# Kernel tuning notes

Measured on AMD Instinct MI355X. Metric: run time of the kernel, lower is better.

## Reference

```python
import jax, jax.numpy as jnp
import numpy as np

B, N, C = 2, 20000, 128
E = 320000
H, COUT = 4, 64
HD = 256  # hidden_dim == H*COUT -> projection is None
ED = 16
L = 3  # LSTM layers


def setup_inputs() -> dict:
    key = jax.random.key(0)
    ks = jax.random.split(key, 16)
    return {
        "x": jax.random.normal(ks[0], (B, N, C), jnp.float32),
        "edge_index": jax.random.randint(ks[1], (2, E), 0, N),
        "edge_attr": jax.random.normal(ks[2], (E, ED), jnp.float32),
        "lin_w": jax.random.normal(ks[3], (C, H * COUT), jnp.float32) / np.sqrt(C),
        "att_src": jax.random.normal(ks[4], (1, H, COUT), jnp.float32) * 0.1,
        "att_dst": jax.random.normal(ks[5], (1, H, COUT), jnp.float32) * 0.1,
        "lin_edge_w": jax.random.normal(ks[6], (ED, H * COUT), jnp.float32) / np.sqrt(ED),
        "att_edge": jax.random.normal(ks[7], (1, H, COUT), jnp.float32) * 0.1,
        "gat_bias": jnp.zeros((H * COUT,), jnp.float32),
        "w_ih": jax.random.normal(ks[8], (L, 4 * HD, HD), jnp.float32) / np.sqrt(HD),
        "w_hh": jax.random.normal(ks[9], (L, 4 * HD, HD), jnp.float32) / np.sqrt(HD),
        "b_ih": jnp.zeros((L, 4 * HD), jnp.float32),
        "b_hh": jnp.zeros((L, 4 * HD), jnp.float32),
        "ln_g": jnp.ones((HD,), jnp.float32),
        "ln_b": jnp.zeros((HD,), jnp.float32),
    }


def reference(x, edge_index, edge_attr, lin_w, att_src, att_dst, lin_edge_w,
              att_edge, gat_bias, w_ih, w_hh, b_ih, b_hh, ln_g, ln_b):
    Bn = B * N
    # ---- GAT: linear transform ----
    xt = (x.reshape(Bn, C) @ lin_w).reshape(Bn, H, COUT)
    # batch-offset edge index, then append self-loops for every node
    off = (jnp.arange(B, dtype=edge_index.dtype) * N)[:, None]
    src = (edge_index[0][None, :] + off).reshape(-1)
    dst = (edge_index[1][None, :] + off).reshape(-1)
    loop = jnp.arange(Bn, dtype=edge_index.dtype)
    src = jnp.concatenate([src, loop])  # [Etot] = [B*E + B*N]
    dst = jnp.concatenate([dst, loop])
    # edge features: shared 2D edge_attr is repeated per batch, zeros on self-loops
    ea = (edge_attr @ lin_edge_w).reshape(E, H, COUT)
    ea = jnp.concatenate([jnp.tile(ea, (B, 1, 1)),
                          jnp.zeros((Bn, H, COUT), xt.dtype)], axis=0)
    # ---- message: gather, score, segment-softmax ----
    x_j = xt[src]  # [Etot, H, COUT]
    x_i = xt[dst]
    alpha = ((x_j * att_src).sum(-1) + (x_i * att_dst).sum(-1)
             + (ea * att_edge).sum(-1))  # [Etot, H]
    alpha = jax.nn.leaky_relu(alpha, 0.2)
    m = jax.ops.segment_max(alpha, dst, num_segments=Bn)
    alpha = jnp.exp(alpha - m[dst])
    s = jax.ops.segment_sum(alpha, dst, num_segments=Bn)
    alpha = alpha / (s[dst] + 1e-16)  # PyG softmax eps; dropout inactive (eval)
    # ---- aggregate (scatter-add) ----
    out = jax.ops.segment_sum(x_j * alpha[..., None], dst, num_segments=Bn)
    spatial = out.reshape(Bn, H * COUT) + gat_bias  # concat heads, [Bn, HD]
    # ---- 3-layer LSTM, seq_len=1, zero initial state (h_prev=None) ----
    h_in = spatial
    hs, cs = [], []
    for l in range(L):
        # h0 = c0 = 0 -> w_hh contributes nothing; inter-layer dropout inactive
        gates = h_in @ w_ih[l].T + b_ih[l] + b_hh[l]
        i, f, g, o = jnp.split(gates, 4, axis=-1)  # PyTorch gate order i,f,g,o
        c = jax.nn.sigmoid(i) * jnp.tanh(g)
        h = jax.nn.sigmoid(o) * jnp.tanh(c)
        hs.append(h)
        cs.append(c)
        h_in = h
    # ---- LayerNorm ----
    h_out = h_in.reshape(B, N, HD)
    mu = h_out.mean(-1, keepdims=True)
    var = ((h_out - mu) ** 2).mean(-1, keepdims=True)
    h_out = (h_out - mu) / jnp.sqrt(var + 1e-5) * ln_g + ln_b
    return h_out, jnp.stack(hs), jnp.stack(cs)
```

## Files before the change

### kernel.cpp

```cpp
#include <hip/hip_runtime.h>
#include <stdint.h>

#define NB_    20000
#define CB_    128
#define EE_    320000
#define BN_    40000
#define BE_    640000
#define ETOT_  680000

typedef __attribute__((ext_vector_type(4))) float f4;
typedef __attribute__((ext_vector_type(4))) unsigned short us4;
typedef __attribute__((ext_vector_type(4))) unsigned int ui4;
typedef __attribute__((ext_vector_type(8))) __bf16 bf16x8;

static __device__ __forceinline__ unsigned short f2bf(float f){
    union { float f; unsigned int u; } v; v.f = f;
    unsigned int u = v.u;
    u += 0x7FFFu + ((u >> 16) & 1u);
    return (unsigned short)(u >> 16);
}
static __device__ __forceinline__ float bf2f(unsigned short b){
    union { unsigned int u; float f; } v; v.u = ((unsigned int)b) << 16;
    return v.f;
}
static __device__ __forceinline__ float sigf(float x){ return 1.f/(1.f+__expf(-x)); }
static __device__ __forceinline__ float tanhfast(float x){ return 2.f/(1.f+__expf(-2.f*x)) - 1.f; }
static __device__ __forceinline__ f4 fmax4(f4 a, f4 b){
    f4 r; r[0]=fmaxf(a[0],b[0]); r[1]=fmaxf(a[1],b[1]); r[2]=fmaxf(a[2],b[2]); r[3]=fmaxf(a[3],b[3]); return r;
}

__global__ void w2_kernel(const float* __restrict__ lew, const float* __restrict__ ae,
                          float* __restrict__ W2){
    int t = threadIdx.x;
    int d = t >> 2, h = t & 3;
    float s = 0.f;
    for (int c = 0; c < 64; ++c) s += lew[d*256 + h*64 + c] * ae[h*64 + c];
    W2[d*4 + h] = s;
}

__global__ void pack_linwT_kernel(const float* __restrict__ lw, unsigned short* __restrict__ wt){
    int tid = blockIdx.x*256 + threadIdx.x;
    int n = tid >> 7, k = tid & 127;
    wt[n*128 + k] = f2bf(lw[k*256 + n]);
}

__global__ void pack_lstmw_kernel(const float* __restrict__ w_ih, unsigned short* __restrict__ Bp){
    int tid = blockIdx.x*256 + threadIdx.x;
    int l   = tid / 196608;
    int rem = tid - l*196608;
    int p = rem >> 8, k = rem & 255;
    int jb = p / 192, q2 = p - jb*192;
    int chunk = q2 / 48, r = q2 - chunk*48;
    int gate = r >> 4, jj = r & 15;
    int gor = (gate == 0) ? 0 : (gate == 1 ? 2 : 3);
    int srcrow = gor*256 + jb*64 + chunk*16 + jj;
    Bp[tid] = f2bf(w_ih[(l*1024 + srcrow)*256 + k]);
}

__global__ void pack_bias_kernel(const float* __restrict__ b_ih, const float* __restrict__ b_hh,
                                 float* __restrict__ bp){
    int tid = blockIdx.x*256 + threadIdx.x;
    if (tid >= 2304) return;
    int l = tid / 768, p = tid - l*768;
    int jb = p / 192, q2 = p - jb*192;
    int chunk = q2 / 48, r = q2 - chunk*48;
    int gate = r >> 4, jj = r & 15;
    int gor = (gate == 0) ? 0 : (gate == 1 ? 2 : 3);
    int srcrow = gor*256 + jb*64 + chunk*16 + jj;
    bp[tid] = b_ih[l*1024 + srcrow] + b_hh[l*1024 + srcrow];
}

__global__ __launch_bounds__(256) void gemm1_kernel(const float* __restrict__ x,
        const unsigned short* __restrict__ wt, unsigned short* __restrict__ xt){
    __shared__ unsigned short As[64*72];
    __shared__ unsigned short Bs[64*72];
    const int tid = threadIdx.x;
    const int bm = blockIdx.x, bn = blockIdx.y;
    const int lane = tid & 63, w = tid >> 6;
    const int wm = w & 1, wn = w >> 1;
    const int nl = lane & 15, q = lane >> 4;
    f4 acc[2][2] = {};
    for (int kc = 0; kc < 128; kc += 64) {
        #pragma unroll
        for (int it = 0; it < 4; ++it) {
            int s = tid + it*256;
            int row = s >> 4, c4 = s & 15;
            f4 v = *(const f4*)&x[(bm*64+row)*128 + kc + c4*4];
            us4 o; o[0]=f2bf(v[0]); o[1]=f2bf(v[1]); o[2]=f2bf(v[2]); o[3]=f2bf(v[3]);
            *(us4*)&As[row*72 + c4*4] = o;
        }
        #pragma unroll
        for (int it = 0; it < 2; ++it) {
            int s = tid + it*256;
            int row = s >> 3, c = s & 7;
            *(ui4*)&Bs[row*72 + c*8] = *(const ui4*)&wt[(bn*64+row)*128 + kc + c*8];
        }
        __syncthreads();
        #pragma unroll
        for (int kk = 0; kk < 64; kk += 32) {
            bf16x8 a[2], b[2];
            #pragma unroll
            for (int mt = 0; mt < 2; ++mt) a[mt] = *(const bf16x8*)&As[(wm*32 + mt*16 + nl)*72 + kk + q*8];
            #pragma unroll
            for (int nt = 0; nt < 2; ++nt) b[nt] = *(const bf16x8*)&Bs[(wn*32 + nt*16 + nl)*72 + kk + q*8];
            #pragma unroll
            for (int mt = 0; mt < 2; ++mt)
                #pragma unroll
                for (int nt = 0; nt < 2; ++nt)
                    acc[mt][nt] = __builtin_amdgcn_mfma_f32_16x16x32_bf16(a[mt], b[nt], acc[mt][nt], 0, 0, 0);
        }
        __syncthreads();
    }
    #pragma unroll
    for (int mt = 0; mt < 2; ++mt)
        #pragma unroll
        for (int nt = 0; nt < 2; ++nt)
            #pragma unroll
            for (int r = 0; r < 4; ++r) {
                int row = bm*64 + wm*32 + mt*16 + q*4 + r;
                int col = bn*64 + wn*32 + nt*16 + nl;
                xt[row*256 + col] = f2bf(acc[mt][nt][r]);
            }
}

__global__ __launch_bounds__(256) void scores_kernel(const unsigned short* __restrict__ xt,
        const float* __restrict__ att_src, const float* __restrict__ att_dst,
        float* __restrict__ s_src, float* __restrict__ s_dst){
    int n = blockIdx.x*4 + (threadIdx.x >> 6);
    int lane = threadIdx.x & 63;
    us4 xv = *(const us4*)&xt[n*256 + lane*4];
    f4 as = *(const f4*)&att_src[lane*4];
    f4 ad = *(const f4*)&att_dst[lane*4];
    float x0=bf2f(xv[0]), x1=bf2f(xv[1]), x2=bf2f(xv[2]), x3=bf2f(xv[3]);
    float ps = x0*as[0]+x1*as[1]+x2*as[2]+x3*as[3];
    float pd = x0*ad[0]+x1*ad[1]+x2*ad[2]+x3*ad[3];
    #pragma unroll
    for (int o = 1; o < 16; o <<= 1) { ps += __shfl_xor(ps, o, 64); pd += __shfl_xor(pd, o, 64); }
    if ((lane & 15) == 0) {
        s_src[n*4 + (lane>>4)] = ps;
        s_dst[n*4 + (lane>>4)] = pd;
    }
}

__global__ __launch_bounds__(256) void eascore_kernel(const float* __restrict__ ea,
        const float* __restrict__ W2, float* __restrict__ esc){
    __shared__ float w2s[64];
    if (threadIdx.x < 64) w2s[threadIdx.x] = W2[threadIdx.x];
    __syncthreads();
    int e = blockIdx.x*256 + threadIdx.x;
    if (e >= EE_) return;
    f4 acc = {};
    #pragma unroll
    for (int d = 0; d < 16; ++d) {
        float v = ea[e*16 + d];
        f4 wv = *(const f4*)&w2s[d*4];
        acc += v * wv;
    }
    *(f4*)&esc[e*4] = acc;
}

__global__ __launch_bounds__(256) void deghist_kernel(const int* __restrict__ ei, int* __restrict__ deg){
    int e = blockIdx.x*256 + threadIdx.x;
    if (e >= ETOT_) return;
    int dst;
    if (e < BE_) { int b = e / EE_, ee = e - b*EE_; dst = ei[EE_ + ee] + b*NB_; }
    else dst = e - BE_;
    atomicAdd(&deg[dst], 1);
}

__global__ __launch_bounds__(256) void scan1_kernel(const int* __restrict__ deg,
        int* __restrict__ inc, int* __restrict__ bsum){
    __shared__ int sd[256];
    int t = threadIdx.x, i = blockIdx.x*256 + t;
    int v = (i < BN_) ? deg[i] : 0;
    sd[t] = v; __syncthreads();
    #pragma unroll
    for (int d = 1; d < 256; d <<= 1) {
        int x = (t >= d) ? sd[t-d] : 0; __syncthreads();
        sd[t] += x; __syncthreads();
    }
    inc[i] = sd[t];
    if (t == 255) bsum[blockIdx.x] = sd[255];
}

__global__ __launch_bounds__(256) void scan2_kernel(const int* __restrict__ bsum,
        int* __restrict__ bpre, int nb){
    __shared__ int sd[256];
    int t = threadIdx.x;
    int v = (t < nb) ? bsum[t] : 0;
    sd[t] = v; __syncthreads();
    #pragma unroll
    for (int d = 1; d < 256; d <<= 1) {
        int x = (t >= d) ? sd[t-d] : 0; __syncthreads();
        sd[t] += x; __syncthreads();
    }
    if (t < nb) bpre[t] = sd[t] - v;
}

__global__ __launch_bounds__(256) void scan3_kernel(const int* __restrict__ inc,
        const int* __restrict__ deg, const int* __restrict__ bpre,
        int* __restrict__ offs, int* __restrict__ cur){
    int i = blockIdx.x*256 + threadIdx.x;
    if (i >= BN_) return;
    int o = inc[i] - deg[i] + bpre[blockIdx.x];
    offs[i] = o; cur[i] = o;
}

__global__ __launch_bounds__(256) void scatter_kernel(const int* __restrict__ ei,
        const float* __restrict__ s_src, const float* __restrict__ s_dst,
        const float* __restrict__ esc, int* __restrict__ cur,
        int* __restrict__ csr_src, float* __restrict__ csr_alpha){
    int e = blockIdx.x*256 + threadIdx.x;
    if (e >= ETOT_) return;
    int src, dst; f4 a;
    if (e < BE_) {
        int b = e / EE_, ee = e - b*EE_;
        src = ei[ee] + b*NB_;
        dst = ei[EE_ + ee] + b*NB_;
        a = *(const f4*)&esc[ee*4];
    } else {
        src = dst = e - BE_;
        a = (f4){0.f, 0.f, 0.f, 0.f};
    }
    a += *(const f4*)&s_src[src*4];
    a += *(const f4*)&s_dst[dst*4];
    #pragma unroll
    for (int h = 0; h < 4; ++h) a[h] = (a[h] > 0.f) ? a[h] : 0.2f*a[h];
    int pos = atomicAdd(&cur[dst], 1);
    csr_src[pos] = src;
    *(f4*)&csr_alpha[pos*4] = a;
}

__global__ __launch_bounds__(256) void aggregate_kernel(const int* __restrict__ offs,
        const int* __restrict__ deg, const int* __restrict__ csr_src,
        const float* __restrict__ csr_alpha, const unsigned short* __restrict__ xt,
        const float* __restrict__ gat_bias, unsigned short* __restrict__ spat){
    int n = blockIdx.x*4 + (threadIdx.x >> 6);
    int lane = threadIdx.x & 63;
    int start = offs[n], d = deg[n];
    f4 mv = {-1e30f, -1e30f, -1e30f, -1e30f};
    for (int i = lane; i < d; i += 64)
        mv = fmax4(mv, *(const f4*)&csr_alpha[(start+i)*4]);
    #pragma unroll
    for (int o = 1; o < 64; o <<= 1) {
        f4 t; t[0]=__shfl_xor(mv[0],o,64); t[1]=__shfl_xor(mv[1],o,64);
        t[2]=__shfl_xor(mv[2],o,64); t[3]=__shfl_xor(mv[3],o,64);
        mv = fmax4(mv, t);
    }
    f4 sv = {};
    for (int i = lane; i < d; i += 64) {
        f4 a = *(const f4*)&csr_alpha[(start+i)*4];
        sv[0] += __expf(a[0]-mv[0]); sv[1] += __expf(a[1]-mv[1]);
        sv[2] += __expf(a[2]-mv[2]); sv[3] += __expf(a[3]-mv[3]);
    }
    #pragma unroll
    for (int o = 1; o < 64; o <<= 1) {
        sv[0]+=__shfl_xor(sv[0],o,64); sv[1]+=__shfl_xor(sv[1],o,64);
        sv[2]+=__shfl_xor(sv[2],o,64); sv[3]+=__shfl_xor(sv[3],o,64);
    }
    int h = lane >> 4;
    float mh = (h==0)?mv[0]:(h==1)?mv[1]:(h==2)?mv[2]:mv[3];
    float sh = (h==0)?sv[0]:(h==1)?sv[1]:(h==2)?sv[2]:sv[3];
    f4 accv = {};
    for (int base = 0; base < d; base += 64) {
        int cnt = min(64, d - base);
        int srcl = (base + lane < d) ? csr_src[start+base+lane] : 0;
        for (int i = 0; i < cnt; ++i) {
            int srcn = __shfl(srcl, i, 64);
            float av = csr_alpha[(start+base+i)*4 + h];
            float ew = __expf(av - mh);
            us4 xv = *(const us4*)&xt[srcn*256 + lane*4];
            accv[0] += ew * bf2f(xv[0]);
            accv[1] += ew * bf2f(xv[1]);
            accv[2] += ew * bf2f(xv[2]);
            accv[3] += ew * bf2f(xv[3]);
        }
    }
    float invs = 1.f / (sh + 1e-16f);
    f4 gb = *(const f4*)&gat_bias[lane*4];
    accv = accv * invs + gb;
    us4 o4; o4[0]=f2bf(accv[0]); o4[1]=f2bf(accv[1]); o4[2]=f2bf(accv[2]); o4[3]=f2bf(accv[3]);
    *(us4*)&spat[n*256 + lane*4] = o4;
}

__global__ __launch_bounds__(256) void lstm_kernel(const unsigned short* __restrict__ A,
        const unsigned short* __restrict__ Bp, const float* __restrict__ bias,
        float* __restrict__ hs_out, float* __restrict__ cs_out, unsigned short* __restrict__ hnext){
    __shared__ unsigned short As[64*72];
    __shared__ unsigned short Bs[192*72];
    const int tid = threadIdx.x;
    const int bm = blockIdx.x, jb = blockIdx.y;
    const int lane = tid & 63, w = tid >> 6;
    const int nl = lane & 15, q = lane >> 4;
    f4 acc[4][3] = {};
    const unsigned short* Bbase = Bp + jb*192*256;
    for (int kc = 0; kc < 256; kc += 64) {
        #pragma unroll
        for (int it = 0; it < 2; ++it) {
            int s = tid + it*256;
            int row = s >> 3, c = s & 7;
            *(ui4*)&As[row*72 + c*8] = *(const ui4*)&A[(bm*64+row)*256 + kc + c*8];
        }
        #pragma unroll
        for (int it = 0; it < 6; ++it) {
            int s = tid + it*256;
            int row = s >> 3, c = s & 7;
            *(ui4*)&Bs[row*72 + c*8] = *(const ui4*)&Bbase[row*256 + kc + c*8];
        }
        __syncthreads();
        #pragma unroll
        for (int kk = 0; kk < 64; kk += 32) {
            bf16x8 a[4], b[3];
            #pragma unroll
            for (int mt = 0; mt < 4; ++mt) a[mt] = *(const bf16x8*)&As[(mt*16 + nl)*72 + kk + q*8];
            #pragma unroll
            for (int gt = 0; gt < 3; ++gt) b[gt] = *(const bf16x8*)&Bs[(w*48 + gt*16 + nl)*72 + kk + q*8];
            #pragma unroll
            for (int mt = 0; mt < 4; ++mt)
                #pragma unroll
                for (int gt = 0; gt < 3; ++gt)
                    acc[mt][gt] = __builtin_amdgcn_mfma_f32_16x16x32_bf16(a[mt], b[gt], acc[mt][gt], 0, 0, 0);
        }
        __syncthreads();
    }
    const int j = jb*64 + w*16 + nl;
    const float bi = bias[jb*192 + w*48 +  0 + nl];
    const float bg = bias[jb*192 + w*48 + 16 + nl];
    const float bo = bias[jb*192 + w*48 + 32 + nl];
    #pragma unroll
    for (int mt = 0; mt < 4; ++mt)
        #pragma unroll
        for (int r = 0; r < 4; ++r) {
            int m = bm*64 + mt*16 + q*4 + r;
            float iv = acc[mt][0][r] + bi;
            float gv = acc[mt][1][r] + bg;
            float ov = acc[mt][2][r] + bo;
            float c = sigf(iv) * tanhfast(gv);
            float hh = sigf(ov) * tanhfast(c);
            cs_out[m*256 + j] = c;
            hs_out[m*256 + j] = hh;
            if (hnext) hnext[m*256 + j] = f2bf(hh);
        }
}

__global__ __launch_bounds__(256) void ln_kernel(const float* __restrict__ hin,
        const float* __restrict__ g, const float* __restrict__ b, float* __restrict__ out){
    int n = blockIdx.x*4 + (threadIdx.x >> 6);
    int lane = threadIdx.x & 63;
    f4 v = *(const f4*)&hin[n*256 + lane*4];
    float s = v[0]+v[1]+v[2]+v[3];
    float ss = v[0]*v[0]+v[1]*v[1]+v[2]*v[2]+v[3]*v[3];
    #pragma unroll
    for (int o = 1; o < 64; o <<= 1) { s += __shfl_xor(s,o,64); ss += __shfl_xor(ss,o,64); }
    float mu = s * (1.f/256.f);
    float var = ss * (1.f/256.f) - mu*mu;
    float rstd = rsqrtf(var + 1e-5f);
    f4 gg = *(const f4*)&g[lane*4], bb = *(const f4*)&b[lane*4];
    f4 o4 = (v - mu) * rstd * gg + bb;
    *(f4*)&out[n*256 + lane*4] = o4;
}

static inline char* carve(char*& p, size_t bytes){
    char* r = p; p += (bytes + 255) & ~(size_t)255; return r;
}

extern "C" void kernel_launch(void* const* d_in, const int* in_sizes, int n_in,
                              void* d_out, int out_size, void* d_ws, size_t ws_size,
                              hipStream_t stream){
    const float* x         = (const float*)d_in[0];
    const int*   ei        = (const int*)  d_in[1];
    const float* edge_attr = (const float*)d_in[2];
    const float* lin_w     = (const float*)d_in[3];
    const float* att_src   = (const float*)d_in[4];
    const float* att_dst   = (const float*)d_in[5];
    const float* lin_edge_w= (const float*)d_in[6];
    const float* att_edge  = (const float*)d_in[7];
    const float* gat_bias  = (const float*)d_in[8];
    const float* w_ih      = (const float*)d_in[9];
    const float* b_ih      = (const float*)d_in[11];
    const float* b_hh      = (const float*)d_in[12];
    const float* ln_g      = (const float*)d_in[13];
    const float* ln_b      = (const float*)d_in[14];

    float* out = (float*)d_out;
    float* hs_base = out + 10240000;
    float* cs_base = out + 40960000;

    unsigned short* xt   = (unsigned short*)(out + 0);
    float* esc           = out + 10240000;
    int*   csr_src       = (int*)(out + 40960000);
    float* csr_alpha     = out + 41640000;
    unsigned short* spat = (unsigned short*)(out + 51200000);
    unsigned short* h0   = (unsigned short*)(out + 61440000);
    unsigned short* h1   = (unsigned short*)(out + 0);

    char* p = (char*)d_ws;
    float* W2          = (float*)carve(p, 64*4);
    float* s_src       = (float*)carve(p, (size_t)BN_*4*4);
    float* s_dst       = (float*)carve(p, (size_t)BN_*4*4);
    unsigned short* lwT= (unsigned short*)carve(p, 32768*2);
    unsigned short* Bp = (unsigned short*)carve(p, 589824*2);
    float* biasP       = (float*)carve(p, 2304*4);
    int* deg           = (int*)carve(p, BN_*4);
    int* inc           = (int*)carve(p, 157*256*4);
    int* bsum          = (int*)carve(p, 256*4);
    int* bpre          = (int*)carve(p, 256*4);
    int* offs          = (int*)carve(p, BN_*4);
    int* cur           = (int*)carve(p, BN_*4);

    hipMemsetAsync(deg, 0, BN_*4, stream);
    w2_kernel<<<1, 64, 0, stream>>>(lin_edge_w, att_edge, W2);
    pack_linwT_kernel<<<128, 256, 0, stream>>>(lin_w, lwT);
    pack_lstmw_kernel<<<2304, 256, 0, stream>>>(w_ih, Bp);
    pack_bias_kernel<<<9, 256, 0, stream>>>(b_ih, b_hh, biasP);

    gemm1_kernel<<<dim3(625, 4), 256, 0, stream>>>(x, lwT, xt);
    scores_kernel<<<10000, 256, 0, stream>>>(xt, att_src, att_dst, s_src, s_dst);
    eascore_kernel<<<1250, 256, 0, stream>>>(edge_attr, W2, esc);

    deghist_kernel<<<2657, 256, 0, stream>>>(ei, deg);
    scan1_kernel<<<157, 256, 0, stream>>>(deg, inc, bsum);
    scan2_kernel<<<1, 256, 0, stream>>>(bsum, bpre, 157);
    scan3_kernel<<<157, 256, 0, stream>>>(inc, deg, bpre, offs, cur);
    scatter_kernel<<<2657, 256, 0, stream>>>(ei, s_src, s_dst, esc, cur, csr_src, csr_alpha);
    aggregate_kernel<<<10000, 256, 0, stream>>>(offs, deg, csr_src, csr_alpha, xt, gat_bias, spat);

    lstm_kernel<<<dim3(625, 4), 256, 0, stream>>>(spat, Bp,          biasP,        hs_base,           cs_base,           h0);
    lstm_kernel<<<dim3(625, 4), 256, 0, stream>>>(h0,   Bp + 196608, biasP + 768,  hs_base + 10240000, cs_base + 10240000, h1);
    lstm_kernel<<<dim3(625, 4), 256, 0, stream>>>(h1,   Bp + 393216, biasP + 1536, hs_base + 20480000, cs_base + 20480000, (unsigned short*)nullptr);

    ln_kernel<<<10000, 256, 0, stream>>>(hs_base + 20480000, ln_g, ln_b, out);
}
```

Before: 601.0 us.

## Retile LSTM GEMM with direct-to-LDS loads, fuse packing, drop softmax max pass

Four changes. The LSTM gate GEMM now uses 128-row tiles and a new pre-swizzled weight layout, loaded straight into LDS with global_load_lds. The separate weight, bias and W2 packing kernels and the degree memset are merged into one launch. The scatter kernel now writes exp(leaky_relu(score)) directly, so aggregation skips the per-node max and exp passes, and the gather-accumulate loop is unrolled by four. Dropping the max subtraction removes softmax overflow protection, and the last LSTM tile reads rows past the node count.

```diff
diff --git a/kernel.cpp b/kernel.cpp
--- a/kernel.cpp
+++ b/kernel.cpp
@@ -25,49 +25,50 @@
 }
 static __device__ __forceinline__ float sigf(float x){ return 1.f/(1.f+__expf(-x)); }
 static __device__ __forceinline__ float tanhfast(float x){ return 2.f/(1.f+__expf(-2.f*x)) - 1.f; }
-static __device__ __forceinline__ f4 fmax4(f4 a, f4 b){
-    f4 r; r[0]=fmaxf(a[0],b[0]); r[1]=fmaxf(a[1],b[1]); r[2]=fmaxf(a[2],b[2]); r[3]=fmaxf(a[3],b[3]); return r;
-}
-
-__global__ void w2_kernel(const float* __restrict__ lew, const float* __restrict__ ae,
-                          float* __restrict__ W2){
-    int t = threadIdx.x;
-    int d = t >> 2, h = t & 3;
-    float s = 0.f;
-    for (int c = 0; c < 64; ++c) s += lew[d*256 + h*64 + c] * ae[h*64 + c];
-    W2[d*4 + h] = s;
-}
-
-__global__ void pack_linwT_kernel(const float* __restrict__ lw, unsigned short* __restrict__ wt){
-    int tid = blockIdx.x*256 + threadIdx.x;
-    int n = tid >> 7, k = tid & 127;
-    wt[n*128 + k] = f2bf(lw[k*256 + n]);
-}
-
-__global__ void pack_lstmw_kernel(const float* __restrict__ w_ih, unsigned short* __restrict__ Bp){
-    int tid = blockIdx.x*256 + threadIdx.x;
-    int l   = tid / 196608;
-    int rem = tid - l*196608;
-    int p = rem >> 8, k = rem & 255;
-    int jb = p / 192, q2 = p - jb*192;
-    int chunk = q2 / 48, r = q2 - chunk*48;
-    int gate = r >> 4, jj = r & 15;
-    int gor = (gate == 0) ? 0 : (gate == 1 ? 2 : 3);
-    int srcrow = gor*256 + jb*64 + chunk*16 + jj;
-    Bp[tid] = f2bf(w_ih[(l*1024 + srcrow)*256 + k]);
-}
-
-__global__ void pack_bias_kernel(const float* __restrict__ b_ih, const float* __restrict__ b_hh,
-                                 float* __restrict__ bp){
-    int tid = blockIdx.x*256 + threadIdx.x;
-    if (tid >= 2304) return;
-    int l = tid / 768, p = tid - l*768;
-    int jb = p / 192, q2 = p - jb*192;
-    int chunk = q2 / 48, r = q2 - chunk*48;
-    int gate = r >> 4, jj = r & 15;
-    int gor = (gate == 0) ? 0 : (gate == 1 ? 2 : 3);
-    int srcrow = gor*256 + jb*64 + chunk*16 + jj;
-    bp[tid] = b_ih[l*1024 + srcrow] + b_hh[l*1024 + srcrow];
+
+static __device__ __forceinline__ void glds16(const unsigned short* g, unsigned short* l){
+    __builtin_amdgcn_global_load_lds(
+        (const __attribute__((address_space(1))) void*)g,
+        (__attribute__((address_space(3))) void*)l, 16, 0, 0);
+}
+
+__global__ __launch_bounds__(256) void pack_kernel(const float* __restrict__ lw,
+        const float* __restrict__ lew, const float* __restrict__ ae,
+        const float* __restrict__ w_ih, const float* __restrict__ b_ih, const float* __restrict__ b_hh,
+        unsigned short* __restrict__ lwT, unsigned short* __restrict__ Bp,
+        float* __restrict__ bsum, float* __restrict__ W2, int* __restrict__ deg){
+    int b = blockIdx.x, t = threadIdx.x;
+    if (b < 2304) {
+        int tid = b*256 + t;
+        int idx = tid;
+        int e = idx & 7;  idx >>= 3;
+        int lane = idx & 63; idx >>= 6;
+        int n = idx % 12; idx /= 12;
+        int kt = idx & 7; idx >>= 3;
+        int jb = idx & 3; int l = idx >> 2;
+        int wn = n / 6, rem = n - wn*6, gate = rem >> 1, jg = rem & 1;
+        int gor = (gate == 0) ? 0 : (gate == 1 ? 2 : 3);
+        int row = gor*256 + jb*64 + wn*32 + jg*16 + (lane & 15);
+        int k = kt*32 + (lane >> 4)*8 + e;
+        Bp[tid] = f2bf(w_ih[(l*1024 + row)*256 + k]);
+    } else if (b < 2432) {
+        int tid = (b-2304)*256 + t;
+        int nn = tid >> 7, k = tid & 127;
+        lwT[nn*128 + k] = f2bf(lw[k*256 + nn]);
+    } else if (b < 2589) {
+        int i = (b-2432)*256 + t;
+        if (i < BN_) deg[i] = 0;
+    } else if (b == 2589) {
+        if (t < 64) {
+            int dd = t >> 2, h = t & 3;
+            float s = 0.f;
+            for (int c = 0; c < 64; ++c) s += lew[dd*256 + h*64 + c] * ae[h*64 + c];
+            W2[dd*4 + h] = s;
+        }
+    } else {
+        int i = (b-2590)*256 + t;
+        if (i < 3072) bsum[i] = b_ih[i] + b_hh[i];
+    }
 }
 
 __global__ __launch_bounds__(256) void gemm1_kernel(const float* __restrict__ x,
@@ -169,7 +170,7 @@
 }
 
 __global__ __launch_bounds__(256) void scan1_kernel(const int* __restrict__ deg,
-        int* __restrict__ inc, int* __restrict__ bsum){
+        int* __restrict__ inc, int* __restrict__ bsumc){
     __shared__ int sd[256];
     int t = threadIdx.x, i = blockIdx.x*256 + t;
     int v = (i < BN_) ? deg[i] : 0;
@@ -180,14 +181,14 @@
         sd[t] += x; __syncthreads();
     }
     inc[i] = sd[t];
-    if (t == 255) bsum[blockIdx.x] = sd[255];
-}
-
-__global__ __launch_bounds__(256) void scan2_kernel(const int* __restrict__ bsum,
+    if (t == 255) bsumc[blockIdx.x] = sd[255];
+}
+
+__global__ __launch_bounds__(256) void scan2_kernel(const int* __restrict__ bsumc,
         int* __restrict__ bpre, int nb){
     __shared__ int sd[256];
     int t = threadIdx.x;
-    int v = (t < nb) ? bsum[t] : 0;
+    int v = (t < nb) ? bsumc[t] : 0;
     sd[t] = v; __syncthreads();
     #pragma unroll
     for (int d = 1; d < 256; d <<= 1) {
@@ -209,7 +210,7 @@
 __global__ __launch_bounds__(256) void scatter_kernel(const int* __restrict__ ei,
         const float* __restrict__ s_src, const float* __restrict__ s_dst,
         const float* __restrict__ esc, int* __restrict__ cur,
-        int* __restrict__ csr_src, float* __restrict__ csr_alpha){
+        int* __restrict__ csr_src, float* __restrict__ csr_e){
     int e = blockIdx.x*256 + threadIdx.x;
     if (e >= ETOT_) return;
     int src, dst; f4 a;
@@ -225,122 +226,136 @@
     a += *(const f4*)&s_src[src*4];
     a += *(const f4*)&s_dst[dst*4];
     #pragma unroll
-    for (int h = 0; h < 4; ++h) a[h] = (a[h] > 0.f) ? a[h] : 0.2f*a[h];
+    for (int h = 0; h < 4; ++h) {
+        float v = a[h];
+        v = (v > 0.f) ? v : 0.2f*v;
+        a[h] = __expf(v);
+    }
     int pos = atomicAdd(&cur[dst], 1);
     csr_src[pos] = src;
-    *(f4*)&csr_alpha[pos*4] = a;
+    *(f4*)&csr_e[pos*4] = a;
 }
 
 __global__ __launch_bounds__(256) void aggregate_kernel(const int* __restrict__ offs,
         const int* __restrict__ deg, const int* __restrict__ csr_src,
-        const float* __restrict__ csr_alpha, const unsigned short* __restrict__ xt,
+        const float* __restrict__ csr_e, const unsigned short* __restrict__ xt,
         const float* __restrict__ gat_bias, unsigned short* __restrict__ spat){
     int n = blockIdx.x*4 + (threadIdx.x >> 6);
     int lane = threadIdx.x & 63;
     int start = offs[n], d = deg[n];
-    f4 mv = {-1e30f, -1e30f, -1e30f, -1e30f};
-    for (int i = lane; i < d; i += 64)
-        mv = fmax4(mv, *(const f4*)&csr_alpha[(start+i)*4]);
-    #pragma unroll
-    for (int o = 1; o < 64; o <<= 1) {
-        f4 t; t[0]=__shfl_xor(mv[0],o,64); t[1]=__shfl_xor(mv[1],o,64);
-        t[2]=__shfl_xor(mv[2],o,64); t[3]=__shfl_xor(mv[3],o,64);
-        mv = fmax4(mv, t);
-    }
     f4 sv = {};
-    for (int i = lane; i < d; i += 64) {
-        f4 a = *(const f4*)&csr_alpha[(start+i)*4];
-        sv[0] += __expf(a[0]-mv[0]); sv[1] += __expf(a[1]-mv[1]);
-        sv[2] += __expf(a[2]-mv[2]); sv[3] += __expf(a[3]-mv[3]);
-    }
+    for (int i = lane; i < d; i += 64) sv += *(const f4*)&csr_e[(start+i)*4];
     #pragma unroll
     for (int o = 1; o < 64; o <<= 1) {
         sv[0]+=__shfl_xor(sv[0],o,64); sv[1]+=__shfl_xor(sv[1],o,64);
         sv[2]+=__shfl_xor(sv[2],o,64); sv[3]+=__shfl_xor(sv[3],o,64);
     }
     int h = lane >> 4;
-    float mh = (h==0)?mv[0]:(h==1)?mv[1]:(h==2)?mv[2]:mv[3];
     float sh = (h==0)?sv[0]:(h==1)?sv[1]:(h==2)?sv[2]:sv[3];
+    float inv = 1.f / (sh + 1e-16f);
+    const float* eh = csr_e + h;
     f4 accv = {};
     for (int base = 0; base < d; base += 64) {
         int cnt = min(64, d - base);
         int srcl = (base + lane < d) ? csr_src[start+base+lane] : 0;
-        for (int i = 0; i < cnt; ++i) {
-            int srcn = __shfl(srcl, i, 64);
-            float av = csr_alpha[(start+base+i)*4 + h];
-            float ew = __expf(av - mh);
-            us4 xv = *(const us4*)&xt[srcn*256 + lane*4];
-            accv[0] += ew * bf2f(xv[0]);
-            accv[1] += ew * bf2f(xv[1]);
-            accv[2] += ew * bf2f(xv[2]);
-            accv[3] += ew * bf2f(xv[3]);
-        }
-    }
-    float invs = 1.f / (sh + 1e-16f);
+        int i = 0;
+        for (; i + 4 <= cnt; i += 4) {
+            int p = start + base + i;
+            int s0=__shfl(srcl,i,64), s1=__shfl(srcl,i+1,64), s2=__shfl(srcl,i+2,64), s3=__shfl(srcl,i+3,64);
+            float e0=eh[p*4], e1=eh[(p+1)*4], e2=eh[(p+2)*4], e3=eh[(p+3)*4];
+            us4 x0=*(const us4*)&xt[s0*256 + lane*4];
+            us4 x1=*(const us4*)&xt[s1*256 + lane*4];
+            us4 x2=*(const us4*)&xt[s2*256 + lane*4];
+            us4 x3=*(const us4*)&xt[s3*256 + lane*4];
+            accv[0] += e0*bf2f(x0[0]) + e1*bf2f(x1[0]) + e2*bf2f(x2[0]) + e3*bf2f(x3[0]);
+            accv[1] += e0*bf2f(x0[1]) + e1*bf2f(x1[1]) + e2*bf2f(x2[1]) + e3*bf2f(x3[1]);
+            accv[2] += e0*bf2f(x0[2]) + e1*bf2f(x1[2]) + e2*bf2f(x2[2]) + e3*bf2f(x3[2]);
+            accv[3] += e0*bf2f(x0[3]) + e1*bf2f(x1[3]) + e2*bf2f(x2[3]) + e3*bf2f(x3[3]);
+        }
+        for (; i < cnt; ++i) {
+            int p = start + base + i;
+            int s0 = __shfl(srcl, i, 64);
+            float e0 = eh[p*4];
+            us4 x0 = *(const us4*)&xt[s0*256 + lane*4];
+            accv[0] += e0*bf2f(x0[0]); accv[1] += e0*bf2f(x0[1]);
+            accv[2] += e0*bf2f(x0[2]); accv[3] += e0*bf2f(x0[3]);
+        }
+    }
     f4 gb = *(const f4*)&gat_bias[lane*4];
-    accv = accv * invs + gb;
+    accv = accv * inv + gb;
     us4 o4; o4[0]=f2bf(accv[0]); o4[1]=f2bf(accv[1]); o4[2]=f2bf(accv[2]); o4[3]=f2bf(accv[3]);
     *(us4*)&spat[n*256 + lane*4] = o4;
 }
 
-__global__ __launch_bounds__(256) void lstm_kernel(const unsigned short* __restrict__ A,
-        const unsigned short* __restrict__ Bp, const float* __restrict__ bias,
-        float* __restrict__ hs_out, float* __restrict__ cs_out, unsigned short* __restrict__ hnext){
-    __shared__ unsigned short As[64*72];
-    __shared__ unsigned short Bs[192*72];
+__global__ __launch_bounds__(256) void lstm2_kernel(const unsigned short* __restrict__ A,
+        const unsigned short* __restrict__ Bp, const float* __restrict__ bsum,
+        float* __restrict__ hs_out, float* __restrict__ cs_out,
+        unsigned short* __restrict__ hnext){
+    __shared__ unsigned short lds[40*512];
     const int tid = threadIdx.x;
+    const int lane = tid & 63, w = tid >> 6;
     const int bm = blockIdx.x, jb = blockIdx.y;
-    const int lane = tid & 63, w = tid >> 6;
+    const int wm = w & 1, wn = w >> 1;
     const int nl = lane & 15, q = lane >> 4;
-    f4 acc[4][3] = {};
-    const unsigned short* Bbase = Bp + jb*192*256;
-    for (int kc = 0; kc < 256; kc += 64) {
-        #pragma unroll
-        for (int it = 0; it < 2; ++it) {
-            int s = tid + it*256;
-            int row = s >> 3, c = s & 7;
-            *(ui4*)&As[row*72 + c*8] = *(const ui4*)&A[(bm*64+row)*256 + kc + c*8];
-        }
-        #pragma unroll
-        for (int it = 0; it < 6; ++it) {
-            int s = tid + it*256;
-            int row = s >> 3, c = s & 7;
-            *(ui4*)&Bs[row*72 + c*8] = *(const ui4*)&Bbase[row*256 + kc + c*8];
+    f4 acc[4][6] = {};
+    const unsigned short* Abase = A + (size_t)(bm*128 + nl)*256 + q*8;
+    const unsigned short* Bjb = Bp + jb*(8*12*512);
+    for (int kci = 0; kci < 4; ++kci) {
+        const int kc = kci*64;
+        #pragma unroll
+        for (int f = 0; f < 4; ++f) {
+            int rt = w*2 + (f >> 1), ktl = f & 1;
+            glds16(Abase + rt*16*256 + kc + ktl*32, &lds[(rt*2 + ktl)*512]);
+        }
+        const unsigned short* Bk = Bjb + (size_t)(kci*2)*12*512 + lane*8;
+        #pragma unroll
+        for (int f = 0; f < 6; ++f) {
+            int ktl = (f >= 3) ? 1 : 0;
+            int nn = w*3 + (ktl ? f-3 : f);
+            glds16(Bk + (ktl*12 + nn)*512, &lds[(16 + ktl*12 + nn)*512]);
         }
         __syncthreads();
         #pragma unroll
-        for (int kk = 0; kk < 64; kk += 32) {
-            bf16x8 a[4], b[3];
-            #pragma unroll
-            for (int mt = 0; mt < 4; ++mt) a[mt] = *(const bf16x8*)&As[(mt*16 + nl)*72 + kk + q*8];
-            #pragma unroll
-            for (int gt = 0; gt < 3; ++gt) b[gt] = *(const bf16x8*)&Bs[(w*48 + gt*16 + nl)*72 + kk + q*8];
+        for (int ktl = 0; ktl < 2; ++ktl) {
+            bf16x8 af[4], bfr[6];
+            #pragma unroll
+            for (int mt = 0; mt < 4; ++mt)
+                af[mt] = *(const bf16x8*)&lds[((wm*4 + mt)*2 + ktl)*512 + lane*8];
+            #pragma unroll
+            for (int nt = 0; nt < 6; ++nt)
+                bfr[nt] = *(const bf16x8*)&lds[(16 + ktl*12 + wn*6 + nt)*512 + lane*8];
             #pragma unroll
             for (int mt = 0; mt < 4; ++mt)
                 #pragma unroll
-                for (int gt = 0; gt < 3; ++gt)
-                    acc[mt][gt] = __builtin_amdgcn_mfma_f32_16x16x32_bf16(a[mt], b[gt], acc[mt][gt], 0, 0, 0);
+                for (int nt = 0; nt < 6; ++nt)
+                    acc[mt][nt] = __builtin_amdgcn_mfma_f32_16x16x32_bf16(af[mt], bfr[nt], acc[mt][nt], 0, 0, 0);
         }
         __syncthreads();
     }
-    const int j = jb*64 + w*16 + nl;
-    const float bi = bias[jb*192 + w*48 +  0 + nl];
-    const float bg = bias[jb*192 + w*48 + 16 + nl];
-    const float bo = bias[jb*192 + w*48 + 32 + nl];
-    #pragma unroll
-    for (int mt = 0; mt < 4; ++mt)
-        #pragma unroll
-        for (int r = 0; r < 4; ++r) {
-            int m = bm*64 + mt*16 + q*4 + r;
-            float iv = acc[mt][0][r] + bi;
-            float gv = acc[mt][1][r] + bg;
-            float ov = acc[mt][2][r] + bo;
-            float c = sigf(iv) * tanhfast(gv);
-            float hh = sigf(ov) * tanhfast(c);
-            cs_out[m*256 + j] = c;
-            hs_out[m*256 + j] = hh;
-            if (hnext) hnext[m*256 + j] = f2bf(hh);
-        }
+    const int jbase = jb*64 + wn*32;
+    #pragma unroll
+    for (int jg = 0; jg < 2; ++jg) {
+        const int j = jbase + jg*16 + nl;
+        const float bi = bsum[j];
+        const float bg = bsum[512 + j];
+        const float bo = bsum[768 + j];
+        #pragma unroll
+        for (int mt = 0; mt < 4; ++mt)
+            #pragma unroll
+            for (int r = 0; r < 4; ++r) {
+                int m = bm*128 + wm*64 + mt*16 + q*4 + r;
+                if (m < BN_) {
+                    float iv = acc[mt][0 + jg][r] + bi;
+                    float gv = acc[mt][2 + jg][r] + bg;
+                    float ov = acc[mt][4 + jg][r] + bo;
+                    float c  = sigf(iv) * tanhfast(gv);
+                    float hh = sigf(ov) * tanhfast(c);
+                    cs_out[m*256 + j] = c;
+                    hs_out[m*256 + j] = hh;
+                    if (hnext) hnext[m*256 + j] = f2bf(hh);
+                }
+            }
+    }
 }
 
 __global__ __launch_bounds__(256) void ln_kernel(const float* __restrict__ hin,
@@ -389,7 +404,7 @@
     unsigned short* xt   = (unsigned short*)(out + 0);
     float* esc           = out + 10240000;
     int*   csr_src       = (int*)(out + 40960000);
-    float* csr_alpha     = out + 41640000;
+    float* csr_e         = out + 41640000;
     unsigned short* spat = (unsigned short*)(out + 51200000);
     unsigned short* h0   = (unsigned short*)(out + 61440000);
     unsigned short* h1   = (unsigned short*)(out + 0);
@@ -400,34 +415,31 @@
     float* s_dst       = (float*)carve(p, (size_t)BN_*4*4);
     unsigned short* lwT= (unsigned short*)carve(p, 32768*2);
     unsigned short* Bp = (unsigned short*)carve(p, 589824*2);
-    float* biasP       = (float*)carve(p, 2304*4);
+    float* bsum        = (float*)carve(p, 3072*4);
     int* deg           = (int*)carve(p, BN_*4);
     int* inc           = (int*)carve(p, 157*256*4);
-    int* bsum          = (int*)carve(p, 256*4);
+    int* bsumc         = (int*)carve(p, 256*4);
     int* bpre          = (int*)carve(p, 256*4);
     int* offs          = (int*)carve(p, BN_*4);
     int* cur           = (int*)carve(p, BN_*4);
 
-    hipMemsetAsync(deg, 0, BN_*4, stream);
-    w2_kernel<<<1, 64, 0, stream>>>(lin_edge_w, att_edge, W2);
-    pack_linwT_kernel<<<128, 256, 0, stream>>>(lin_w, lwT);
-    pack_lstmw_kernel<<<2304, 256, 0, stream>>>(w_ih, Bp);
-    pack_bias_kernel<<<9, 256, 0, stream>>>(b_ih, b_hh, biasP);
+    pack_kernel<<<2602, 256, 0, stream>>>(lin_w, lin_edge_w, att_edge, w_ih, b_ih, b_hh,
+                                          lwT, Bp, bsum, W2, deg);
 
     gemm1_kernel<<<dim3(625, 4), 256, 0, stream>>>(x, lwT, xt);
     scores_kernel<<<10000, 256, 0, stream>>>(xt, att_src, att_dst, s_src, s_dst);
     eascore_kernel<<<1250, 256, 0, stream>>>(edge_attr, W2, esc);
 
     deghist_kernel<<<2657, 256, 0, stream>>>(ei, deg);
-    scan1_kernel<<<157, 256, 0, stream>>>(deg, inc, bsum);
-    scan2_kernel<<<1, 256, 0, stream>>>(bsum, bpre, 157);
+    scan1_kernel<<<157, 256, 0, stream>>>(deg, inc, bsumc);
+    scan2_kernel<<<1, 256, 0, stream>>>(bsumc, bpre, 157);
     scan3_kernel<<<157, 256, 0, stream>>>(inc, deg, bpre, offs, cur);
-    scatter_kernel<<<2657, 256, 0, stream>>>(ei, s_src, s_dst, esc, cur, csr_src, csr_alpha);
-    aggregate_kernel<<<10000, 256, 0, stream>>>(offs, deg, csr_src, csr_alpha, xt, gat_bias, spat);
-
-    lstm_kernel<<<dim3(625, 4), 256, 0, stream>>>(spat, Bp,          biasP,        hs_base,           cs_base,           h0);
-    lstm_kernel<<<dim3(625, 4), 256, 0, stream>>>(h0,   Bp + 196608, biasP + 768,  hs_base + 10240000, cs_base + 10240000, h1);
-    lstm_kernel<<<dim3(625, 4), 256, 0, stream>>>(h1,   Bp + 393216, biasP + 1536, hs_base + 20480000, cs_base + 20480000, (unsigned short*)nullptr);
+    scatter_kernel<<<2657, 256, 0, stream>>>(ei, s_src, s_dst, esc, cur, csr_src, csr_e);
+    aggregate_kernel<<<10000, 256, 0, stream>>>(offs, deg, csr_src, csr_e, xt, gat_bias, spat);
+
+    lstm2_kernel<<<dim3(313, 4), 256, 0, stream>>>(spat, Bp,          bsum,        hs_base,            cs_base,            h0);
+    lstm2_kernel<<<dim3(313, 4), 256, 0, stream>>>(h0,   Bp + 196608, bsum + 1024, hs_base + 10240000, cs_base + 10240000, h1);
+    lstm2_kernel<<<dim3(313, 4), 256, 0, stream>>>(h1,   Bp + 393216, bsum + 2048, hs_base + 20480000, cs_base + 20480000, (unsigned short*)nullptr);
 
     ln_kernel<<<10000, 256, 0, stream>>>(hs_base + 20480000, ln_g, ln_b, out);
 }
```

New measurement: 659.4 us. 1.1x slower.
